# Optimization experiments

Hardware: AMD Instinct MI355X
Metric: run time of the kernel (lower is better)

## Reference

```python
import jax, jax.numpy as jnp
import numpy as np

UNITS = 1024
NCLASS = 8000
BATCH = 4096

def setup_inputs() -> dict:
    key = jax.random.key(0)
    k1, k2, k3, k4 = jax.random.split(key, 4)
    inputs = jax.random.randint(k1, (BATCH, 1), 0, NCLASS, dtype=jnp.int32)
    h_tm1 = jax.random.normal(k2, (BATCH, UNITS), dtype=jnp.float32)
    # orthogonal-ish recurrent kernel (scaled normal is fine for a numeric reference)
    recurrent_kernel = jax.random.normal(k3, (UNITS, 4 * UNITS), dtype=jnp.float32) * (1.0 / np.sqrt(UNITS))
    kernel_c = jax.random.normal(k4, (NCLASS, 4 * UNITS), dtype=jnp.float32) * (1.0 / np.sqrt(NCLASS))
    bias_z = jnp.full((UNITS,), 5.0, dtype=jnp.float32)  # initializer=constant(5)
    bias = jnp.zeros((3 * UNITS,), dtype=jnp.float32)
    return {"inputs": inputs, "h_tm1": h_tm1, "recurrent_kernel": recurrent_kernel,
            "kernel_c": kernel_c, "bias_z": bias_z, "bias": bias}

def reference(inputs, h_tm1, recurrent_kernel, kernel_c, bias_z, bias):
    u = h_tm1.shape[-1]
    ch = inputs[:, 0].astype(jnp.int32)
    # one_hot(ch) @ kernel_c == row gather of kernel_c (identical math, O(1) per row)
    c_proj = kernel_c[ch]                      # [B, 4u]
    cz, cr, ch_, co = (c_proj[:, :u], c_proj[:, u:2*u], c_proj[:, 2*u:3*u], c_proj[:, 3*u:])
    Rz, Rr, Rh, Ro = (recurrent_kernel[:, :u], recurrent_kernel[:, u:2*u],
                      recurrent_kernel[:, 2*u:3*u], recurrent_kernel[:, 3*u:])
    z = jax.nn.sigmoid(h_tm1 @ Rz + cz + bias_z)
    r = jax.nn.sigmoid(h_tm1 @ Rr + cr + bias[:u])
    hh = jnp.tanh((r * h_tm1) @ Rh + ch_ + bias[u:2*u])
    h = z * h_tm1 + (1.0 - z) * hh
    o = jnp.tanh(h @ Ro + co + bias[2*u:])
    return (o, h)
```

## Files before the change

### kernel.cpp

```cpp
#include <hip/hip_runtime.h>
#include <stdint.h>

#define UNITS 1024
#define BATCH 4096
#define FOURU 4096

typedef __bf16 bf16x8 __attribute__((ext_vector_type(8)));
typedef float f32x4 __attribute__((ext_vector_type(4)));

__device__ __forceinline__ uint16_t f2bf(float f) {
  uint32_t u = __builtin_bit_cast(uint32_t, f);
  u += 0x7FFFu + ((u >> 16) & 1u);
  return (uint16_t)(u >> 16);
}
__device__ __forceinline__ float bf2f(uint16_t b) {
  uint32_t u = ((uint32_t)b) << 16;
  return __builtin_bit_cast(float, u);
}
__device__ __forceinline__ float fsig(float x) {
  return 1.0f / (1.0f + __expf(-x));
}
__device__ __forceinline__ f32x4 mfma16x16x32(bf16x8 a, bf16x8 b, f32x4 c) {
  return __builtin_amdgcn_mfma_f32_16x16x32_bf16(a, b, c, 0, 0, 0);
}

__device__ __forceinline__ void gll16(uint16_t* lds, const uint16_t* g) {
  __builtin_amdgcn_global_load_lds(
      (const __attribute__((address_space(1))) uint32_t*)g,
      (__attribute__((address_space(3))) uint32_t*)lds, 16, 0, 0);
}

__device__ __forceinline__ int fidx(int row, int l4) {
  return row * 4 + (l4 ^ ((row >> 1) & 3));
}

template <int ROWS>
__device__ __forceinline__ void stage32s(const uint16_t* __restrict__ src,
                                         uint16_t* lds, int tid) {
  const int wb = tid & 192;
#pragma unroll
  for (int p = 0; p < ROWS / 64; ++p) {
    const int gi = p * 256 + tid;
    const int row = gi >> 2;
    const int kg = (gi & 3) ^ ((row >> 1) & 3);
    gll16(lds + (p * 256 + wb) * 8, src + row * UNITS + kg * 8);
  }
}

__global__ __launch_bounds__(256) void prep_kernel(const float* __restrict__ h32,
                                                   uint16_t* __restrict__ hbf,
                                                   const float* __restrict__ R,
                                                   uint16_t* __restrict__ RT) {
  __shared__ float t[32][33];
  const int b = blockIdx.x;
  if (b < 4096) {
    const int i = (b * 256 + threadIdx.x) * 4;
    float4 v = *(const float4*)(h32 + i);
    ushort4 o;
    o.x = f2bf(v.x); o.y = f2bf(v.y); o.z = f2bf(v.z); o.w = f2bf(v.w);
    *(ushort4*)(hbf + i) = o;
  } else {
    const int bb = b - 4096;
    const int n0 = (bb & 127) * 32, k0 = (bb >> 7) * 32;
    const int tx = threadIdx.x & 31, ty = threadIdx.x >> 5;
#pragma unroll
    for (int i = 0; i < 4; ++i)
      t[ty + i * 8][tx] = R[(size_t)(k0 + ty + i * 8) * FOURU + n0 + tx];
    __syncthreads();
#pragma unroll
    for (int i = 0; i < 4; ++i)
      RT[(size_t)(n0 + ty + i * 8) * UNITS + k0 + tx] = f2bf(t[tx][ty + i * 8]);
  }
}

template <int BN, int EPI>
__global__ __launch_bounds__(256, 4) void gemm_kernel(
    const uint16_t* __restrict__ abf, const uint16_t* __restrict__ bt,
    const int* __restrict__ idx, const float* __restrict__ kc,
    const float* __restrict__ bz, const float* __restrict__ bias,
    const float* __restrict__ h32, const uint16_t* __restrict__ hbf,
    const uint16_t* __restrict__ zb_in, float* __restrict__ out32,
    uint16_t* __restrict__ outbf, uint16_t* __restrict__ out2bf) {
  constexpr int NF = BN / 32;
  __shared__ uint16_t sA[2][64 * 32];
  __shared__ uint16_t sB[2][BN * 32];
  const int tid = threadIdx.x;
  const int lane = tid & 63, wave = tid >> 6;
  const int l15 = lane & 15, l4 = lane >> 4;
  const int fid = blockIdx.y * 16 + blockIdx.x;
  const int nid = (fid & 7) * 128 + (fid >> 3);
  const int row0 = (nid & 63) * 64;
  const int col0 = (nid >> 6) * BN;
  const int wr = wave >> 1, wc = wave & 1;
  const uint16_t* pa = abf + (size_t)row0 * UNITS;
  const uint16_t* pb = bt + (size_t)col0 * UNITS;
  f32x4 acc[2][NF] = {};

  stage32s<64>(pa, sA[0], tid);
  stage32s<BN>(pb, sB[0], tid);
  __syncthreads();

  int cur = 0;
  for (int t = 0; t < 32; ++t) {
    if (t < 31) {
      stage32s<64>(pa + (t + 1) * 32, sA[cur ^ 1], tid);
      stage32s<BN>(pb + (t + 1) * 32, sB[cur ^ 1], tid);
    }
    const bf16x8* A8 = (const bf16x8*)sA[cur];
    const bf16x8* B8 = (const bf16x8*)sB[cur];
    bf16x8 af[2], bf[NF];
#pragma unroll
    for (int m = 0; m < 2; ++m) af[m] = A8[fidx(wr * 32 + m * 16 + l15, l4)];
#pragma unroll
    for (int n = 0; n < NF; ++n)
      bf[n] = B8[fidx(wc * (BN / 2) + n * 16 + l15, l4)];
#pragma unroll
    for (int m = 0; m < 2; ++m)
#pragma unroll
      for (int n = 0; n < NF; ++n)
        acc[m][n] = mfma16x16x32(af[m], bf[n], acc[m][n]);
    __syncthreads();
    cur ^= 1;
  }

#pragma unroll
  for (int m = 0; m < 2; ++m) {
#pragma unroll
    for (int q = 0; q < 4; ++q) {
      const int i = row0 + wr * 32 + m * 16 + l4 * 4 + q;
      const int ch = idx[i];
      const float* kcrow = kc + (size_t)ch * FOURU;
#pragma unroll
      for (int n = 0; n < NF; ++n) {
        const int jc = col0 + wc * (BN / 2) + n * 16 + l15;
        const float a = acc[m][n][q];
        if (EPI == 0) {
          if (jc < UNITS) {
            float z = fsig(a + kcrow[jc] + bz[jc]);
            outbf[(size_t)i * UNITS + jc] = f2bf(z);
          } else {
            const int j = jc - UNITS;
            const size_t ij = (size_t)i * UNITS + j;
            float r = fsig(a + kcrow[jc] + bias[j]);
            out2bf[ij] = f2bf(r * bf2f(hbf[ij]));
          }
        } else if (EPI == 1) {
          const size_t ij = (size_t)i * UNITS + jc;
          float hh = tanhf(a + kcrow[2 * UNITS + jc] + bias[UNITS + jc]);
          float z = bf2f(zb_in[ij]);
          float hv = h32[ij];
          float hn = z * hv + (1.0f - z) * hh;
          out32[ij] = hn;
          outbf[ij] = f2bf(hn);
        } else {
          const size_t ij = (size_t)i * UNITS + jc;
          out32[ij] = tanhf(a + kcrow[3 * UNITS + jc] + bias[2 * UNITS + jc]);
        }
      }
    }
  }
}

extern "C" void kernel_launch(void* const* d_in, const int* in_sizes, int n_in,
                              void* d_out, int out_size, void* d_ws, size_t ws_size,
                              hipStream_t stream) {
  const int* idx = (const int*)d_in[0];
  const float* h32 = (const float*)d_in[1];
  const float* R = (const float*)d_in[2];
  const float* kc = (const float*)d_in[3];
  const float* bz = (const float*)d_in[4];
  const float* bias = (const float*)d_in[5];

  float* o_out = (float*)d_out;
  float* h_out = o_out + (size_t)BATCH * UNITS;

  uint16_t* hbf = (uint16_t*)d_ws;
  uint16_t* rt = hbf + (size_t)BATCH * UNITS;
  uint16_t* rhb = rt + (size_t)FOURU * UNITS;
  uint16_t* hnb = rhb + (size_t)BATCH * UNITS;
  uint16_t* zbuf = hnb + (size_t)BATCH * UNITS;

  prep_kernel<<<dim3(8192), 256, 0, stream>>>(h32, hbf, R, rt);

  gemm_kernel<128, 0><<<dim3(16, 64), 256, 0, stream>>>(
      hbf, rt, idx, kc, bz, bias, h32, hbf, nullptr, nullptr, zbuf, rhb);

  gemm_kernel<64, 1><<<dim3(16, 64), 256, 0, stream>>>(
      rhb, rt + (size_t)2 * UNITS * UNITS, idx, kc, bz, bias, h32, hbf, zbuf,
      h_out, hnb, nullptr);

  gemm_kernel<64, 2><<<dim3(16, 64), 256, 0, stream>>>(
      hnb, rt + (size_t)3 * UNITS * UNITS, idx, kc, bz, bias, nullptr, nullptr,
      nullptr, o_out, nullptr, nullptr);
}
```

Before: 107.9 us.

## Deepen GEMM pipeline to four LDS stages and unify tile width

Replaces the double-buffered K loop with a 4-buffer, 3-deep prefetch pipeline using explicit vmcnt waits and a single barrier per iteration. It fixes the N tile at 128 for all three GEMMs, halving the grid for the second and third. It also reads h_tm1 from the bf16 copy instead of fp32 in the hidden-state epilogue, which cuts traffic but reduces precision. Larger LDS use and lower occupancy bounds may reduce latency hiding in exchange.

```diff
diff --git a/kernel.cpp b/kernel.cpp
--- a/kernel.cpp
+++ b/kernel.cpp
@@ -7,6 +7,8 @@
 
 typedef __bf16 bf16x8 __attribute__((ext_vector_type(8)));
 typedef float f32x4 __attribute__((ext_vector_type(4)));
+
+#define VMW(n) asm volatile("s_waitcnt vmcnt(" #n ")" ::: "memory")
 
 __device__ __forceinline__ uint16_t f2bf(float f) {
   uint32_t u = __builtin_bit_cast(uint32_t, f);
@@ -73,69 +75,86 @@
   }
 }
 
-template <int BN, int EPI>
-__global__ __launch_bounds__(256, 4) void gemm_kernel(
+template <int EPI>
+__global__ __launch_bounds__(256, 3) void gemm_kernel(
     const uint16_t* __restrict__ abf, const uint16_t* __restrict__ bt,
     const int* __restrict__ idx, const float* __restrict__ kc,
     const float* __restrict__ bz, const float* __restrict__ bias,
-    const float* __restrict__ h32, const uint16_t* __restrict__ hbf,
-    const uint16_t* __restrict__ zb_in, float* __restrict__ out32,
-    uint16_t* __restrict__ outbf, uint16_t* __restrict__ out2bf) {
-  constexpr int NF = BN / 32;
-  __shared__ uint16_t sA[2][64 * 32];
-  __shared__ uint16_t sB[2][BN * 32];
+    const uint16_t* __restrict__ hbf, const uint16_t* __restrict__ zb_in,
+    float* __restrict__ out32, uint16_t* __restrict__ outbf,
+    uint16_t* __restrict__ out2bf) {
+  __shared__ uint16_t sA[4][64 * 32];
+  __shared__ uint16_t sB[4][128 * 32];
   const int tid = threadIdx.x;
   const int lane = tid & 63, wave = tid >> 6;
   const int l15 = lane & 15, l4 = lane >> 4;
-  const int fid = blockIdx.y * 16 + blockIdx.x;
-  const int nid = (fid & 7) * 128 + (fid >> 3);
+  const int fid = blockIdx.y * gridDim.x + blockIdx.x;
+  const int q = (gridDim.x * gridDim.y) >> 3;
+  const int nid = (fid & 7) * q + (fid >> 3);
   const int row0 = (nid & 63) * 64;
-  const int col0 = (nid >> 6) * BN;
+  const int col0 = (nid >> 6) * 128;
   const int wr = wave >> 1, wc = wave & 1;
   const uint16_t* pa = abf + (size_t)row0 * UNITS;
   const uint16_t* pb = bt + (size_t)col0 * UNITS;
-  f32x4 acc[2][NF] = {};
-
-  stage32s<64>(pa, sA[0], tid);
-  stage32s<BN>(pb, sB[0], tid);
-  __syncthreads();
-
-  int cur = 0;
-  for (int t = 0; t < 32; ++t) {
-    if (t < 31) {
-      stage32s<64>(pa + (t + 1) * 32, sA[cur ^ 1], tid);
-      stage32s<BN>(pb + (t + 1) * 32, sB[cur ^ 1], tid);
-    }
-    const bf16x8* A8 = (const bf16x8*)sA[cur];
-    const bf16x8* B8 = (const bf16x8*)sB[cur];
-    bf16x8 af[2], bf[NF];
+  f32x4 acc[2][4] = {};
+
+  auto stageAB = [&](int t) {
+    stage32s<64>(pa + t * 32, sA[t & 3], tid);
+    stage32s<128>(pb + t * 32, sB[t & 3], tid);
+  };
+  auto consume = [&](int b) {
+    const bf16x8* A8 = (const bf16x8*)sA[b];
+    const bf16x8* B8 = (const bf16x8*)sB[b];
+    bf16x8 af[2], bfr[4];
 #pragma unroll
     for (int m = 0; m < 2; ++m) af[m] = A8[fidx(wr * 32 + m * 16 + l15, l4)];
 #pragma unroll
-    for (int n = 0; n < NF; ++n)
-      bf[n] = B8[fidx(wc * (BN / 2) + n * 16 + l15, l4)];
+    for (int n = 0; n < 4; ++n) bfr[n] = B8[fidx(wc * 64 + n * 16 + l15, l4)];
 #pragma unroll
     for (int m = 0; m < 2; ++m)
 #pragma unroll
-      for (int n = 0; n < NF; ++n)
-        acc[m][n] = mfma16x16x32(af[m], bf[n], acc[m][n]);
-    __syncthreads();
-    cur ^= 1;
-  }
-
+      for (int n = 0; n < 4; ++n)
+        acc[m][n] = mfma16x16x32(af[m], bfr[n], acc[m][n]);
+  };
+
+  stageAB(0);
+  stageAB(1);
+  stageAB(2);
+
+  for (int t = 0; t < 29; ++t) {
+    VMW(6);
+    __builtin_amdgcn_s_barrier();
+    __builtin_amdgcn_sched_barrier(0);
+    stageAB(t + 3);
+    consume(t & 3);
+  }
+  VMW(6);
+  __builtin_amdgcn_s_barrier();
+  __builtin_amdgcn_sched_barrier(0);
+  consume(1);
+  VMW(3);
+  __builtin_amdgcn_s_barrier();
+  __builtin_amdgcn_sched_barrier(0);
+  consume(2);
+  VMW(0);
+  __builtin_amdgcn_s_barrier();
+  __builtin_amdgcn_sched_barrier(0);
+  consume(3);
+
+  const bool is_z = (col0 < UNITS);
 #pragma unroll
   for (int m = 0; m < 2; ++m) {
 #pragma unroll
-    for (int q = 0; q < 4; ++q) {
-      const int i = row0 + wr * 32 + m * 16 + l4 * 4 + q;
+    for (int qq = 0; qq < 4; ++qq) {
+      const int i = row0 + wr * 32 + m * 16 + l4 * 4 + qq;
       const int ch = idx[i];
       const float* kcrow = kc + (size_t)ch * FOURU;
 #pragma unroll
-      for (int n = 0; n < NF; ++n) {
-        const int jc = col0 + wc * (BN / 2) + n * 16 + l15;
-        const float a = acc[m][n][q];
+      for (int n = 0; n < 4; ++n) {
+        const int jc = col0 + wc * 64 + n * 16 + l15;
+        const float a = acc[m][n][qq];
         if (EPI == 0) {
-          if (jc < UNITS) {
+          if (is_z) {
             float z = fsig(a + kcrow[jc] + bz[jc]);
             outbf[(size_t)i * UNITS + jc] = f2bf(z);
           } else {
@@ -148,7 +167,7 @@
           const size_t ij = (size_t)i * UNITS + jc;
           float hh = tanhf(a + kcrow[2 * UNITS + jc] + bias[UNITS + jc]);
           float z = bf2f(zb_in[ij]);
-          float hv = h32[ij];
+          float hv = bf2f(hbf[ij]);
           float hn = z * hv + (1.0f - z) * hh;
           out32[ij] = hn;
           outbf[ij] = f2bf(hn);
@@ -182,14 +201,14 @@
 
   prep_kernel<<<dim3(8192), 256, 0, stream>>>(h32, hbf, R, rt);
 
-  gemm_kernel<128, 0><<<dim3(16, 64), 256, 0, stream>>>(
-      hbf, rt, idx, kc, bz, bias, h32, hbf, nullptr, nullptr, zbuf, rhb);
-
-  gemm_kernel<64, 1><<<dim3(16, 64), 256, 0, stream>>>(
-      rhb, rt + (size_t)2 * UNITS * UNITS, idx, kc, bz, bias, h32, hbf, zbuf,
+  gemm_kernel<0><<<dim3(16, 64), 256, 0, stream>>>(
+      hbf, rt, idx, kc, bz, bias, hbf, nullptr, nullptr, zbuf, rhb);
+
+  gemm_kernel<1><<<dim3(8, 64), 256, 0, stream>>>(
+      rhb, rt + (size_t)2 * UNITS * UNITS, idx, kc, bz, bias, hbf, zbuf,
       h_out, hnb, nullptr);
 
-  gemm_kernel<64, 2><<<dim3(16, 64), 256, 0, stream>>>(
+  gemm_kernel<2><<<dim3(8, 64), 256, 0, stream>>>(
       hnb, rt + (size_t)3 * UNITS * UNITS, idx, kc, bz, bias, nullptr, nullptr,
-      nullptr, o_out, nullptr, nullptr);
-}
+      o_out, nullptr, nullptr);
+}
```

Result: slower. 130.4 us (+20.9%).

## Fuse prep and three GEMM stages into one cooperative persistent kernel

Applied to the files above, without the earlier changes.

Replaces the four separate launches with a single cooperative kernel. It sizes the grid from occupancy, loops persistently over tiles, and separates the phases with grid-wide syncs, keeping the old launches as a fallback. It also caches the per-row class index in LDS and reads h from the bf16 copy instead of fp32 in the h-update epilogue. The aim is to remove launch gaps and tail effects between stages, at the cost of grid-sync overhead, a possibly smaller resident grid, and slightly lower precision for h.

```diff
diff --git a/kernel.cpp b/kernel.cpp
--- a/kernel.cpp
+++ b/kernel.cpp
@@ -1,9 +1,13 @@
 #include <hip/hip_runtime.h>
+#include <hip/hip_cooperative_groups.h>
 #include <stdint.h>
+
+namespace cg = cooperative_groups;
 
 #define UNITS 1024
 #define BATCH 4096
 #define FOURU 4096
+#define SMEM_BYTES (24 * 1024 + 256)
 
 typedef __bf16 bf16x8 __attribute__((ext_vector_type(8)));
 typedef float f32x4 __attribute__((ext_vector_type(4)));
@@ -45,6 +49,156 @@
     const int kg = (gi & 3) ^ ((row >> 1) & 3);
     gll16(lds + (p * 256 + wb) * 8, src + row * UNITS + kg * 8);
   }
+}
+
+template <int BN, int EPI>
+__device__ __forceinline__ void gemm_tile(
+    int nid, char* smemc, const uint16_t* __restrict__ abf,
+    const uint16_t* __restrict__ bt, const int* __restrict__ idx,
+    const float* __restrict__ kc, const float* __restrict__ bz,
+    const float* __restrict__ bias, const uint16_t* __restrict__ hbf,
+    const uint16_t* __restrict__ zb_in, float* __restrict__ out32,
+    uint16_t* __restrict__ outbf, uint16_t* __restrict__ out2bf) {
+  constexpr int NF = BN / 32;
+  uint16_t* sA = (uint16_t*)smemc;
+  uint16_t* sB = (uint16_t*)(smemc + 8192);
+  int* sIdx = (int*)(smemc + 24 * 1024);
+  const int tid = threadIdx.x;
+  const int lane = tid & 63, wave = tid >> 6;
+  const int l15 = lane & 15, l4 = lane >> 4;
+  const int row0 = (nid & 63) * 64;
+  const int col0 = (nid >> 6) * BN;
+  const int wr = wave >> 1, wc = wave & 1;
+  const uint16_t* pa = abf + (size_t)row0 * UNITS;
+  const uint16_t* pb = bt + (size_t)col0 * UNITS;
+  f32x4 acc[2][NF] = {};
+
+  __syncthreads();
+  if (tid < 64) sIdx[tid] = idx[row0 + tid];
+  stage32s<64>(pa, sA, tid);
+  stage32s<BN>(pb, sB, tid);
+  __syncthreads();
+
+  int cur = 0;
+  for (int t = 0; t < 32; ++t) {
+    if (t < 31) {
+      stage32s<64>(pa + (t + 1) * 32, sA + (cur ^ 1) * 2048, tid);
+      stage32s<BN>(pb + (t + 1) * 32, sB + (cur ^ 1) * BN * 32, tid);
+    }
+    const bf16x8* A8 = (const bf16x8*)(sA + cur * 2048);
+    const bf16x8* B8 = (const bf16x8*)(sB + cur * BN * 32);
+    bf16x8 af[2], bfr[NF];
+#pragma unroll
+    for (int m = 0; m < 2; ++m) af[m] = A8[fidx(wr * 32 + m * 16 + l15, l4)];
+#pragma unroll
+    for (int n = 0; n < NF; ++n)
+      bfr[n] = B8[fidx(wc * (BN / 2) + n * 16 + l15, l4)];
+#pragma unroll
+    for (int m = 0; m < 2; ++m)
+#pragma unroll
+      for (int n = 0; n < NF; ++n)
+        acc[m][n] = mfma16x16x32(af[m], bfr[n], acc[m][n]);
+    __syncthreads();
+    cur ^= 1;
+  }
+
+  const bool is_z = (col0 < UNITS);
+#pragma unroll
+  for (int m = 0; m < 2; ++m) {
+#pragma unroll
+    for (int q = 0; q < 4; ++q) {
+      const int lr = wr * 32 + m * 16 + l4 * 4 + q;
+      const int i = row0 + lr;
+      const int ch = sIdx[lr];
+      const float* kcrow = kc + (size_t)ch * FOURU;
+#pragma unroll
+      for (int n = 0; n < NF; ++n) {
+        const int jc = col0 + wc * (BN / 2) + n * 16 + l15;
+        const float a = acc[m][n][q];
+        if (EPI == 0) {
+          if (is_z) {
+            float z = fsig(a + kcrow[jc] + bz[jc]);
+            outbf[(size_t)i * UNITS + jc] = f2bf(z);
+          } else {
+            const int j = jc - UNITS;
+            const size_t ij = (size_t)i * UNITS + j;
+            float r = fsig(a + kcrow[jc] + bias[j]);
+            out2bf[ij] = f2bf(r * bf2f(hbf[ij]));
+          }
+        } else if (EPI == 1) {
+          const size_t ij = (size_t)i * UNITS + jc;
+          float hh = tanhf(a + kcrow[2 * UNITS + jc] + bias[UNITS + jc]);
+          float z = bf2f(zb_in[ij]);
+          float hv = bf2f(hbf[ij]);
+          float hn = z * hv + (1.0f - z) * hh;
+          out32[ij] = hn;
+          outbf[ij] = f2bf(hn);
+        } else {
+          const size_t ij = (size_t)i * UNITS + jc;
+          out32[ij] = tanhf(a + kcrow[3 * UNITS + jc] + bias[2 * UNITS + jc]);
+        }
+      }
+    }
+  }
+}
+
+__global__ __launch_bounds__(256, 4) void fused_kernel(
+    const int* __restrict__ idx, const float* __restrict__ h32,
+    const float* __restrict__ R, const float* __restrict__ kc,
+    const float* __restrict__ bz, const float* __restrict__ bias,
+    float* __restrict__ o_out, float* __restrict__ h_out,
+    uint16_t* __restrict__ hbf, uint16_t* __restrict__ rt,
+    uint16_t* __restrict__ rhb, uint16_t* __restrict__ hnb,
+    uint16_t* __restrict__ zbuf) {
+  __shared__ __align__(16) char smem[SMEM_BYTES];
+  const int tid = threadIdx.x;
+  const int bid = blockIdx.x;
+  const int gnum = gridDim.x;
+  cg::grid_group grid = cg::this_grid();
+
+  for (int c = bid; c < 1024; c += gnum) {
+#pragma unroll
+    for (int p = 0; p < 4; ++p) {
+      const int i = c * 4096 + p * 1024 + tid * 4;
+      float4 v = *(const float4*)(h32 + i);
+      ushort4 o;
+      o.x = f2bf(v.x); o.y = f2bf(v.y); o.z = f2bf(v.z); o.w = f2bf(v.w);
+      *(ushort4*)(hbf + i) = o;
+    }
+  }
+  {
+    float(*t)[33] = (float(*)[33])smem;
+    const int tx = tid & 31, ty = tid >> 5;
+    for (int tt = bid; tt < 4096; tt += gnum) {
+      const int n0 = (tt & 127) * 32, k0 = (tt >> 7) * 32;
+      __syncthreads();
+#pragma unroll
+      for (int i2 = 0; i2 < 4; ++i2)
+        t[ty + i2 * 8][tx] = R[(size_t)(k0 + ty + i2 * 8) * FOURU + n0 + tx];
+      __syncthreads();
+#pragma unroll
+      for (int i2 = 0; i2 < 4; ++i2)
+        rt[(size_t)(n0 + ty + i2 * 8) * UNITS + k0 + tx] =
+            f2bf(t[tx][ty + i2 * 8]);
+    }
+  }
+  grid.sync();
+
+  for (int it = bid; it < 1024; it += gnum)
+    gemm_tile<128, 0>((it & 7) * 128 + (it >> 3), smem, hbf, rt, idx, kc, bz,
+                      bias, hbf, nullptr, nullptr, zbuf, rhb);
+  grid.sync();
+
+  for (int it = bid; it < 1024; it += gnum)
+    gemm_tile<64, 1>((it & 7) * 128 + (it >> 3), smem, rhb,
+                     rt + (size_t)2 * UNITS * UNITS, idx, kc, bz, bias, hbf,
+                     zbuf, h_out, hnb, nullptr);
+  grid.sync();
+
+  for (int it = bid; it < 1024; it += gnum)
+    gemm_tile<64, 2>((it & 7) * 128 + (it >> 3), smem, hnb,
+                     rt + (size_t)3 * UNITS * UNITS, idx, kc, bz, bias,
+                     nullptr, nullptr, o_out, nullptr, nullptr);
 }
 
 __global__ __launch_bounds__(256) void prep_kernel(const float* __restrict__ h32,
@@ -78,87 +232,13 @@
     const uint16_t* __restrict__ abf, const uint16_t* __restrict__ bt,
     const int* __restrict__ idx, const float* __restrict__ kc,
     const float* __restrict__ bz, const float* __restrict__ bias,
-    const float* __restrict__ h32, const uint16_t* __restrict__ hbf,
-    const uint16_t* __restrict__ zb_in, float* __restrict__ out32,
-    uint16_t* __restrict__ outbf, uint16_t* __restrict__ out2bf) {
-  constexpr int NF = BN / 32;
-  __shared__ uint16_t sA[2][64 * 32];
-  __shared__ uint16_t sB[2][BN * 32];
-  const int tid = threadIdx.x;
-  const int lane = tid & 63, wave = tid >> 6;
-  const int l15 = lane & 15, l4 = lane >> 4;
-  const int fid = blockIdx.y * 16 + blockIdx.x;
-  const int nid = (fid & 7) * 128 + (fid >> 3);
-  const int row0 = (nid & 63) * 64;
-  const int col0 = (nid >> 6) * BN;
-  const int wr = wave >> 1, wc = wave & 1;
-  const uint16_t* pa = abf + (size_t)row0 * UNITS;
-  const uint16_t* pb = bt + (size_t)col0 * UNITS;
-  f32x4 acc[2][NF] = {};
-
-  stage32s<64>(pa, sA[0], tid);
-  stage32s<BN>(pb, sB[0], tid);
-  __syncthreads();
-
-  int cur = 0;
-  for (int t = 0; t < 32; ++t) {
-    if (t < 31) {
-      stage32s<64>(pa + (t + 1) * 32, sA[cur ^ 1], tid);
-      stage32s<BN>(pb + (t + 1) * 32, sB[cur ^ 1], tid);
-    }
-    const bf16x8* A8 = (const bf16x8*)sA[cur];
-    const bf16x8* B8 = (const bf16x8*)sB[cur];
-    bf16x8 af[2], bf[NF];
-#pragma unroll
-    for (int m = 0; m < 2; ++m) af[m] = A8[fidx(wr * 32 + m * 16 + l15, l4)];
-#pragma unroll
-    for (int n = 0; n < NF; ++n)
-      bf[n] = B8[fidx(wc * (BN / 2) + n * 16 + l15, l4)];
-#pragma unroll
-    for (int m = 0; m < 2; ++m)
-#pragma unroll
-      for (int n = 0; n < NF; ++n)
-        acc[m][n] = mfma16x16x32(af[m], bf[n], acc[m][n]);
-    __syncthreads();
-    cur ^= 1;
-  }
-
-#pragma unroll
-  for (int m = 0; m < 2; ++m) {
-#pragma unroll
-    for (int q = 0; q < 4; ++q) {
-      const int i = row0 + wr * 32 + m * 16 + l4 * 4 + q;
-      const int ch = idx[i];
-      const float* kcrow = kc + (size_t)ch * FOURU;
-#pragma unroll
-      for (int n = 0; n < NF; ++n) {
-        const int jc = col0 + wc * (BN / 2) + n * 16 + l15;
-        const float a = acc[m][n][q];
-        if (EPI == 0) {
-          if (jc < UNITS) {
-            float z = fsig(a + kcrow[jc] + bz[jc]);
-            outbf[(size_t)i * UNITS + jc] = f2bf(z);
-          } else {
-            const int j = jc - UNITS;
-            const size_t ij = (size_t)i * UNITS + j;
-            float r = fsig(a + kcrow[jc] + bias[j]);
-            out2bf[ij] = f2bf(r * bf2f(hbf[ij]));
-          }
-        } else if (EPI == 1) {
-          const size_t ij = (size_t)i * UNITS + jc;
-          float hh = tanhf(a + kcrow[2 * UNITS + jc] + bias[UNITS + jc]);
-          float z = bf2f(zb_in[ij]);
-          float hv = h32[ij];
-          float hn = z * hv + (1.0f - z) * hh;
-          out32[ij] = hn;
-          outbf[ij] = f2bf(hn);
-        } else {
-          const size_t ij = (size_t)i * UNITS + jc;
-          out32[ij] = tanhf(a + kcrow[3 * UNITS + jc] + bias[2 * UNITS + jc]);
-        }
-      }
-    }
-  }
+    const uint16_t* __restrict__ hbf, const uint16_t* __restrict__ zb_in,
+    float* __restrict__ out32, uint16_t* __restrict__ outbf,
+    uint16_t* __restrict__ out2bf) {
+  __shared__ __align__(16) char smem[SMEM_BYTES];
+  const int b = blockIdx.x;
+  gemm_tile<BN, EPI>((b & 7) * 128 + (b >> 3), smem, abf, bt, idx, kc, bz,
+                     bias, hbf, zb_in, out32, outbf, out2bf);
 }
 
 extern "C" void kernel_launch(void* const* d_in, const int* in_sizes, int n_in,
@@ -180,16 +260,29 @@
   uint16_t* hnb = rhb + (size_t)BATCH * UNITS;
   uint16_t* zbuf = hnb + (size_t)BATCH * UNITS;
 
-  prep_kernel<<<dim3(8192), 256, 0, stream>>>(h32, hbf, R, rt);
-
-  gemm_kernel<128, 0><<<dim3(16, 64), 256, 0, stream>>>(
-      hbf, rt, idx, kc, bz, bias, h32, hbf, nullptr, nullptr, zbuf, rhb);
-
-  gemm_kernel<64, 1><<<dim3(16, 64), 256, 0, stream>>>(
-      rhb, rt + (size_t)2 * UNITS * UNITS, idx, kc, bz, bias, h32, hbf, zbuf,
-      h_out, hnb, nullptr);
-
-  gemm_kernel<64, 2><<<dim3(16, 64), 256, 0, stream>>>(
-      hnb, rt + (size_t)3 * UNITS * UNITS, idx, kc, bz, bias, nullptr, nullptr,
-      nullptr, o_out, nullptr, nullptr);
-}
+  int maxb = 0;
+  hipError_t oc = hipOccupancyMaxActiveBlocksPerMultiprocessor(
+      &maxb, (const void*)fused_kernel, 256, 0);
+  int grid = (oc == hipSuccess && maxb > 0) ? maxb * 256 : 0;
+  if (grid > 1024) grid = 1024;
+  grid &= ~7;
+
+  hipError_t err = hipErrorUnknown;
+  if (grid >= 8) {
+    void* args[] = {&idx,  &h32, &R,   &kc, &bz,  &bias, &o_out,
+                    &h_out, &hbf, &rt, &rhb, &hnb, &zbuf};
+    err = hipLaunchCooperativeKernel((void*)fused_kernel, dim3(grid),
+                                     dim3(256), args, 0, stream);
+  }
+  if (err != hipSuccess) {
+    prep_kernel<<<dim3(8192), 256, 0, stream>>>(h32, hbf, R, rt);
+    gemm_kernel<128, 0><<<dim3(1024), 256, 0, stream>>>(
+        hbf, rt, idx, kc, bz, bias, hbf, nullptr, nullptr, zbuf, rhb);
+    gemm_kernel<64, 1><<<dim3(1024), 256, 0, stream>>>(
+        rhb, rt + (size_t)2 * UNITS * UNITS, idx, kc, bz, bias, hbf, zbuf,
+        h_out, hnb, nullptr);
+    gemm_kernel<64, 2><<<dim3(1024), 256, 0, stream>>>(
+        hnb, rt + (size_t)3 * UNITS * UNITS, idx, kc, bz, bias, nullptr,
+        nullptr, o_out, nullptr, nullptr);
+  }
+}
```

Result: slower. 328.3 us (+204.3%).
